# Optimization experiments

Hardware: AMD Instinct MI355X
Metric: run time of the kernel (lower is better)

Reference implementation:

```python
import jax, jax.numpy as jnp
import numpy as np


def bilinear_resize(x, out_h, out_w):
    # x: [B, C, H, W]; matches torch F.interpolate(mode='bilinear', align_corners=False)
    B, C, H, W = x.shape
    ry = jnp.clip((jnp.arange(out_h, dtype=jnp.float32) + 0.5) * (H / out_h) - 0.5, 0.0, H - 1)
    rx = jnp.clip((jnp.arange(out_w, dtype=jnp.float32) + 0.5) * (W / out_w) - 0.5, 0.0, W - 1)
    y0 = jnp.floor(ry).astype(jnp.int32); y1 = jnp.minimum(y0 + 1, H - 1)
    x0 = jnp.floor(rx).astype(jnp.int32); x1 = jnp.minimum(x0 + 1, W - 1)
    wy = (ry - y0)[:, None]  # [out_h,1]
    wx = (rx - x0)[None, :]  # [1,out_w]
    r0 = x[:, :, y0, :]; r1 = x[:, :, y1, :]
    v00 = r0[:, :, :, x0]; v01 = r0[:, :, :, x1]
    v10 = r1[:, :, :, x0]; v11 = r1[:, :, :, x1]
    return (v00 * (1 - wx) + v01 * wx) * (1 - wy) + (v10 * (1 - wx) + v11 * wx) * wy


def setup_inputs() -> dict:
    key0 = jax.random.key(0)
    ks = jax.random.split(key0, 16)
    B, N, C, H = 2, 300, 256, 8
    hw_lvl = np.array([[64, 64], [32, 32], [16, 16]], dtype=np.int64)
    L = int((hw_lvl[:, 0] * hw_lvl[:, 1]).sum())  # 5376
    p = lambda k, sh: (0.02 * jax.random.normal(k, sh, dtype=jnp.float32))
    return {
        'query': jax.random.normal(ks[0], (B, N, C), dtype=jnp.float32),
        'key': jax.random.normal(ks[1], (B, L, C), dtype=jnp.float32),
        'value': jax.random.normal(ks[2], (B, L, C), dtype=jnp.float32),
        'key_padding_mask': jnp.zeros((B, L), dtype=bool),
        'hw_lvl': hw_lvl,
        'Wq': p(ks[3], (C, C)), 'Wk': p(ks[4], (C, C)), 'Wv': p(ks[5], (C, C)),
        'Wp': p(ks[6], (C, C)), 'bp': jnp.zeros((C,), jnp.float32),
        'W1': p(ks[7], (H, H)), 'b1': jnp.zeros((H,), jnp.float32),
        'W2': p(ks[8], (H, H)), 'b2': jnp.zeros((H,), jnp.float32),
        'W3': p(ks[9], (H, H)), 'b3': jnp.zeros((H,), jnp.float32),
        'Wm': p(ks[10], (3 * H, 1)), 'bm': jnp.zeros((1,), jnp.float32),
    }


def reference(query, key, value, key_padding_mask, hw_lvl,
              Wq, Wk, Wv, Wp, bp, W1, b1, W2, b2, W3, b3, Wm, bm):
    hw = np.asarray(hw_lvl)
    h1, wd1 = int(hw[0, 0]), int(hw[0, 1])
    h2, wd2 = int(hw[1, 0]), int(hw[1, 1])
    h3, wd3 = int(hw[2, 0]), int(hw[2, 1])
    w1 = h1 * wd1
    w2 = w1 + h2 * wd2
    B, N, C = query.shape
    L = key.shape[1]
    H = W1.shape[0]
    scale = (C // H) ** -0.5

    q = (query @ Wq).reshape(B, N, H, C // H)
    k = (key @ Wk).reshape(B, L, H, C // H)
    v = (value @ Wv).reshape(B, L, H, C // H)
    attn = jnp.einsum('bnhd,blhd->bhnl', q, k) * scale  # [B,H,N,L]

    ap = attn.transpose(0, 2, 3, 1)  # [B,N,L,H]
    f1 = jax.nn.relu(ap[:, :, :w1] @ W1 + b1)                      # [B,N,w1,H]
    f2 = jax.nn.relu(ap[:, :, w1:w2] @ W2 + b2)                    # [B,N,h2*wd2,H]
    f3 = jax.nn.relu(ap[:, :, w2:] @ W3 + b3)                      # [B,N,h3*wd3,H]
    f2 = f2.transpose(0, 1, 3, 2).reshape(B * N, H, h2, wd2)
    f3 = f3.transpose(0, 1, 3, 2).reshape(B * N, H, h3, wd3)
    f2 = bilinear_resize(f2, h1, wd1).transpose(0, 2, 3, 1).reshape(B, N, w1, H)
    f3 = bilinear_resize(f3, h1, wd1).transpose(0, 2, 3, 1).reshape(B, N, w1, H)
    new_feats = jnp.concatenate([f1, f2, f3], axis=-1)             # [B,N,w1,3H]
    mask = jax.nn.relu(new_feats @ Wm + bm)                        # [B,N,w1,1]

    aw = jax.nn.softmax(attn, axis=-1)                             # [B,H,N,L]
    x = jnp.einsum('bhnl,blhd->bnhd', aw, v).reshape(B, N, C)
    x = x @ Wp + bp
    return x, mask
```

## Files before the change

### kernel.cpp

```cpp
#include <hip/hip_runtime.h>
#include <hip/hip_bf16.h>

typedef __hip_bfloat16 bf16;
typedef __attribute__((ext_vector_type(8))) short short8v;
typedef __attribute__((ext_vector_type(8))) unsigned short ushort8v;
typedef __attribute__((ext_vector_type(4))) unsigned short ushort4v;
typedef __attribute__((ext_vector_type(4))) float float4v;

__device__ __forceinline__ float bfu2f(unsigned short u) {
    union { unsigned int i; float f; } v; v.i = ((unsigned int)u) << 16; return v.f;
}
__device__ __forceinline__ unsigned short f2bfu_rn(float x) {
    union { float f; unsigned int i; } u; u.f = x;
    unsigned int r = (u.i + 0x7FFFu + ((u.i >> 16) & 1u)) >> 16;
    return (unsigned short)r;
}

__global__ __launch_bounds__(256) void cast_wt(
    const float* __restrict__ Wq, const float* __restrict__ Wk,
    const float* __restrict__ Wv, const float* __restrict__ Wp,
    unsigned short* __restrict__ wt)
{
    __shared__ unsigned short tile[64][72];
    const float* W = (blockIdx.z == 0) ? Wq : (blockIdx.z == 1) ? Wk
                   : (blockIdx.z == 2) ? Wv : Wp;
    unsigned short* WT = wt + (size_t)blockIdx.z * 65536;
    const int t = threadIdx.x;
    const int k0 = blockIdx.x * 64, n0 = blockIdx.y * 64;
    {
        const int r = t >> 2, cseg = (t & 3) * 16;
        const float* src = W + (size_t)(k0 + r) * 256 + n0 + cseg;
        #pragma unroll
        for (int j = 0; j < 16; ++j) tile[r][cseg + j] = f2bfu_rn(src[j]);
    }
    __syncthreads();
    {
        const int ch = t & 63, lq = t >> 6;
        ushort8v o0, o1;
        #pragma unroll
        for (int i = 0; i < 8; ++i) o0[i] = tile[lq * 16 + i][ch];
        #pragma unroll
        for (int i = 0; i < 8; ++i) o1[i] = tile[lq * 16 + 8 + i][ch];
        unsigned short* dst = WT + (size_t)(n0 + ch) * 256 + k0 + lq * 16;
        *(ushort8v*)(dst)     = o0;
        *(ushort8v*)(dst + 8) = o1;
    }
}

__device__ __forceinline__ void proj_core(
    const float* __restrict__ aptr, const unsigned short* __restrict__ Wt,
    int nc0, int m16, int quad, float4v acc[8])
{
    #pragma unroll
    for (int i = 0; i < 8; ++i) acc[i] = (float4v){0.f, 0.f, 0.f, 0.f};
    #pragma unroll
    for (int ks = 0; ks < 8; ++ks) {
        float4 a0 = *(const float4*)(aptr + ks * 32);
        float4 a1 = *(const float4*)(aptr + ks * 32 + 4);
        short8v af;
        af[0] = (short)f2bfu_rn(a0.x); af[1] = (short)f2bfu_rn(a0.y);
        af[2] = (short)f2bfu_rn(a0.z); af[3] = (short)f2bfu_rn(a0.w);
        af[4] = (short)f2bfu_rn(a1.x); af[5] = (short)f2bfu_rn(a1.y);
        af[6] = (short)f2bfu_rn(a1.z); af[7] = (short)f2bfu_rn(a1.w);
        #pragma unroll
        for (int i = 0; i < 8; ++i) {
            short8v bfr = *(const short8v*)(Wt + (size_t)(nc0 + i * 16 + m16) * 256 + ks * 32 + quad * 8);
            acc[i] = __builtin_amdgcn_mfma_f32_16x16x32_bf16(af, bfr, acc[i], 0, 0, 0);
        }
    }
}

__global__ __launch_bounds__(256) void proj_all(
    const float* __restrict__ q, const float* __restrict__ k, const float* __restrict__ v,
    const unsigned short* __restrict__ wt,
    unsigned short* __restrict__ qb, unsigned short* __restrict__ kb,
    unsigned short* __restrict__ vt)
{
    const int t = threadIdx.x;
    const int wave = t >> 6, lane = t & 63;
    const int m16 = lane & 15, quad = lane >> 4;
    const int msub = (wave & 1) * 16;
    const int nc0 = (wave >> 1) * 128;
    const int bx = blockIdx.x;

    float4v acc[8];
    if (bx < 19) {
        const int m0 = bx * 32;
        const int arow = min(m0 + msub + m16, 599);
        proj_core(q + (size_t)arow * 256 + quad * 8, wt, nc0, m16, quad, acc);
        #pragma unroll
        for (int i = 0; i < 8; ++i)
            #pragma unroll
            for (int r = 0; r < 4; ++r) {
                int m = m0 + msub + quad * 4 + r;
                if (m < 600)
                    qb[(size_t)m * 256 + nc0 + i * 16 + m16] = f2bfu_rn(acc[i][r]);
            }
    } else if (bx < 355) {
        const int m0 = (bx - 19) * 32;
        proj_core(k + (size_t)(m0 + msub + m16) * 256 + quad * 8, wt + 65536, nc0, m16, quad, acc);
        #pragma unroll
        for (int i = 0; i < 8; ++i)
            #pragma unroll
            for (int r = 0; r < 4; ++r) {
                int m = m0 + msub + quad * 4 + r;
                kb[(size_t)m * 256 + nc0 + i * 16 + m16] = f2bfu_rn(acc[i][r]);
            }
    } else {
        const int m0 = (bx - 355) * 32;
        proj_core(v + (size_t)(m0 + msub + m16) * 256 + quad * 8, wt + 131072, nc0, m16, quad, acc);
        const int bb = (m0 >= 5376) ? 1 : 0;
        const int lcol = m0 - bb * 5376 + msub + quad * 4;
        #pragma unroll
        for (int i = 0; i < 8; ++i) {
            const int ch = nc0 + i * 16 + m16;
            ushort4v p;
            #pragma unroll
            for (int r = 0; r < 4; ++r) p[r] = f2bfu_rn(acc[i][r]);
            *(ushort4v*)(vt + (size_t)(bb * 256 + ch) * 5376 + lcol) = p;
        }
    }
}

__global__ __launch_bounds__(256) void proj_out(
    const float* __restrict__ xb, const unsigned short* __restrict__ Wtp,
    const float* __restrict__ bp, float* __restrict__ out)
{
    const int t = threadIdx.x;
    const int wave = t >> 6, lane = t & 63;
    const int m16 = lane & 15, quad = lane >> 4;
    const int msub = (wave & 1) * 16;
    const int nc0 = (wave >> 1) * 128;
    const int m0 = blockIdx.x * 32;

    const int arow = min(m0 + msub + m16, 599);
    float4v acc[8];
    proj_core(xb + (size_t)arow * 256 + quad * 8, Wtp, nc0, m16, quad, acc);

    #pragma unroll
    for (int i = 0; i < 8; ++i) {
        const float bv = bp[nc0 + i * 16 + m16];
        #pragma unroll
        for (int r = 0; r < 4; ++r) {
            int m = m0 + msub + quad * 4 + r;
            if (m < 600)
                out[(size_t)m * 256 + nc0 + i * 16 + m16] = acc[i][r] + bv;
        }
    }
}

__global__ __launch_bounds__(512) void attn_fused(
    const unsigned short* __restrict__ qb, const unsigned short* __restrict__ kb,
    const unsigned short* __restrict__ vt,
    unsigned short* __restrict__ attn, float* __restrict__ xb)
{
    __shared__ unsigned short probs[8][16 * 232];
    __shared__ float partial[8][64][9];
    __shared__ float SrowP[8][16];

    const int t = threadIdx.x;
    const int wave = t >> 6, lane = t & 63;
    const int n0 = blockIdx.x * 16;
    const int bh = blockIdx.y;
    const int b = bh >> 3, h = bh & 7;
    const int m16 = lane & 15, quad = lane >> 4;
    const float scale = 0.17677669529663687f;

    const unsigned short* qp = qb + (size_t)(b * 300 + min(n0 + m16, 299)) * 256 + h * 32 + quad * 8;
    const short8v qfrag = *(const short8v*)qp;

    const unsigned short* kbase = kb + (size_t)(b * 5376) * 256 + h * 32 + quad * 8;
    const unsigned short* vt0 = vt + (size_t)(b * 256 + h * 32 + m16) * 5376;
    const unsigned short* vt1 = vt0 + (size_t)16 * 5376;

    unsigned short* pw = &probs[wave][0];
    const int lwave = wave * 672;

    float4v c0 = {0.f, 0.f, 0.f, 0.f};
    float4v c1 = {0.f, 0.f, 0.f, 0.f};
    float sm = 0.f;

    for (int cch = 0; cch < 3; ++cch) {
        const int lc = lwave + cch * 224;

        for (int i = 0; i < 14; ++i) {
            const int lcol = lc + i * 16 + m16;
            short8v kf = *(const short8v*)(kbase + (size_t)lcol * 256);
            float4v c = {0.f, 0.f, 0.f, 0.f};
            c = __builtin_amdgcn_mfma_f32_16x16x32_bf16(kf, qfrag, c, 0, 0, 0);
            ushort4v pk;
            #pragma unroll
            for (int r = 0; r < 4; ++r) pk[r] = f2bfu_rn(c[r] * scale);
            *(ushort4v*)(pw + m16 * 232 + i * 16 + quad * 4) = pk;
        }

        {
            const int row = lane >> 2;
            const int n = n0 + row;
            if (n < 300) {
                unsigned short* gdst = attn + ((size_t)(b * 300 + n) * 8 + h) * 5376 + lc;
                const unsigned short* lsrc = pw + row * 232;
                #pragma unroll
                for (int it = 0; it < 7; ++it) {
                    const int colk = (lane & 3) * 8 + it * 32;
                    *(ushort8v*)(gdst + colk) = *(const ushort8v*)(lsrc + colk);
                }
            }
        }

        for (int step = 0; step < 7; ++step) {
            const int lloc = step * 32 + quad * 8;
            ushort8v ua = *(const ushort8v*)(pw + m16 * 232 + lloc);
            short8v af;
            #pragma unroll
            for (int j = 0; j < 8; ++j) {
                float e = __expf(bfu2f(ua[j]));
                sm += e;
                af[j] = (short)f2bfu_rn(e);
            }
            const int lg = lc + lloc;
            short8v b0 = *(const short8v*)(vt0 + lg);
            short8v b1 = *(const short8v*)(vt1 + lg);
            c0 = __builtin_amdgcn_mfma_f32_16x16x32_bf16(af, b0, c0, 0, 0, 0);
            c1 = __builtin_amdgcn_mfma_f32_16x16x32_bf16(af, b1, c1, 0, 0, 0);
        }
    }

    sm += __shfl_xor(sm, 16);
    sm += __shfl_xor(sm, 32);
    if (lane < 16) SrowP[wave][lane] = sm;
    #pragma unroll
    for (int j = 0; j < 4; ++j) {
        partial[wave][lane][j]     = c0[j];
        partial[wave][lane][4 + j] = c1[j];
    }
    __syncthreads();

    if (t < 64) {
        float acc[8] = {0.f, 0.f, 0.f, 0.f, 0.f, 0.f, 0.f, 0.f};
        #pragma unroll
        for (int w = 0; w < 8; ++w)
            #pragma unroll
            for (int j = 0; j < 8; ++j) acc[j] += partial[w][t][j];

        const int d = t & 15, q = t >> 4;
        #pragma unroll
        for (int r = 0; r < 4; ++r) {
            const int row = q * 4 + r;
            const int nn = n0 + row;
            if (nn < 300) {
                float S = 0.f;
                #pragma unroll
                for (int w = 0; w < 8; ++w) S += SrowP[w][row];
                float* o = xb + (size_t)(b * 300 + nn) * 256 + h * 32 + d;
                o[0]  = acc[r] / S;
                o[16] = acc[4 + r] / S;
            }
        }
    }
}

__global__ __launch_bounds__(256) void mask_kernel(
    const bf16* __restrict__ attn,
    const float* __restrict__ W1, const float* __restrict__ b1,
    const float* __restrict__ W2, const float* __restrict__ b2,
    const float* __restrict__ W3, const float* __restrict__ b3,
    const float* __restrict__ Wm, const float* __restrict__ bmp,
    float* __restrict__ out)
{
    __shared__ float g2s[1024];
    __shared__ float g3s[256];
    __shared__ float w1s[64], w2s[64], w3s[64];
    __shared__ float b1s[8], b2s[8], b3s[8];
    __shared__ float wms[24];
    __shared__ float bms;

    const int t  = threadIdx.x;
    const int bn = blockIdx.x;
    const int ph = blockIdx.y;
    const unsigned short* ap = (const unsigned short*)attn + (size_t)bn * 8 * 5376;

    if (t < 64) { w1s[t] = W1[t]; w2s[t] = W2[t]; w3s[t] = W3[t]; }
    if (t < 8)  { b1s[t] = b1[t]; b2s[t] = b2[t]; b3s[t] = b3[t]; }
    if (t < 24) wms[t] = Wm[t];
    if (t == 0) bms = bmp[0];
    __syncthreads();

    {
        const int l2 = t * 4;
        ushort4v u[8];
        #pragma unroll
        for (int hh = 0; hh < 8; ++hh)
            u[hh] = *(const ushort4v*)(ap + hh * 5376 + 4096 + l2);
        #pragma unroll
        for (int pp = 0; pp < 4; ++pp) {
            float g = 0.f;
            #pragma unroll
            for (int hh = 0; hh < 8; ++hh) {
                float s = b2s[hh];
                #pragma unroll
                for (int hp = 0; hp < 8; ++hp) s += bfu2f(u[hp][pp]) * w2s[hp * 8 + hh];
                g += fmaxf(s, 0.f) * wms[8 + hh];
            }
            g2s[l2 + pp] = g;
        }
    }
    if (t < 64) {
        const int l3 = t * 4;
        ushort4v u[8];
        #pragma unroll
        for (int hh = 0; hh < 8; ++hh)
            u[hh] = *(const ushort4v*)(ap + hh * 5376 + 5120 + l3);
        #pragma unroll
        for (int pp = 0; pp < 4; ++pp) {
            float g = 0.f;
            #pragma unroll
            for (int hh = 0; hh < 8; ++hh) {
                float s = b3s[hh];
                #pragma unroll
                for (int hp = 0; hp < 8; ++hp) s += bfu2f(u[hp][pp]) * w3s[hp * 8 + hh];
                g += fmaxf(s, 0.f) * wms[16 + hh];
            }
            g3s[l3 + pp] = g;
        }
    }
    __syncthreads();

    {
        const int p0 = ph * 2048 + t * 8;
        ushort8v u[8];
        #pragma unroll
        for (int hh = 0; hh < 8; ++hh)
            u[hh] = *(const ushort8v*)(ap + hh * 5376 + p0);

        float res[8];
        #pragma unroll
        for (int pp = 0; pp < 8; ++pp) {
            const int p = p0 + pp;
            const int Y = p >> 6, X = p & 63;

            float acc = bms;
            #pragma unroll
            for (int hh = 0; hh < 8; ++hh) {
                float s = b1s[hh];
                #pragma unroll
                for (int hp = 0; hp < 8; ++hp) s += bfu2f(u[hp][pp]) * w1s[hp * 8 + hh];
                acc += fmaxf(s, 0.f) * wms[hh];
            }
            {
                float ry = fminf(fmaxf(0.5f * Y - 0.25f, 0.f), 31.f);
                float rx = fminf(fmaxf(0.5f * X - 0.25f, 0.f), 31.f);
                int y0 = (int)ry, x0 = (int)rx;
                int y1 = min(y0 + 1, 31), x1 = min(x0 + 1, 31);
                float wy = ry - (float)y0, wx = rx - (float)x0;
                acc += (g2s[y0 * 32 + x0] * (1.f - wx) + g2s[y0 * 32 + x1] * wx) * (1.f - wy)
                     + (g2s[y1 * 32 + x0] * (1.f - wx) + g2s[y1 * 32 + x1] * wx) * wy;
            }
            {
                float ry = fminf(fmaxf(0.25f * Y - 0.375f, 0.f), 15.f);
                float rx = fminf(fmaxf(0.25f * X - 0.375f, 0.f), 15.f);
                int y0 = (int)ry, x0 = (int)rx;
                int y1 = min(y0 + 1, 15), x1 = min(x0 + 1, 15);
                float wy = ry - (float)y0, wx = rx - (float)x0;
                acc += (g3s[y0 * 16 + x0] * (1.f - wx) + g3s[y0 * 16 + x1] * wx) * (1.f - wy)
                     + (g3s[y1 * 16 + x0] * (1.f - wx) + g3s[y1 * 16 + x1] * wx) * wy;
            }
            res[pp] = fmaxf(acc, 0.f);
        }
        float* o = out + 153600 + (size_t)bn * 4096 + p0;
        #pragma unroll
        for (int pp = 0; pp < 8; ++pp) o[pp] = res[pp];
    }
}

extern "C" void kernel_launch(void* const* d_in, const int* in_sizes, int n_in,
                              void* d_out, int out_size, void* d_ws, size_t ws_size,
                              hipStream_t stream) {
    const float* query = (const float*)d_in[0];
    const float* key   = (const float*)d_in[1];
    const float* value = (const float*)d_in[2];
    const float* Wq = (const float*)d_in[5];
    const float* Wk = (const float*)d_in[6];
    const float* Wv = (const float*)d_in[7];
    const float* Wp = (const float*)d_in[8];
    const float* bp = (const float*)d_in[9];
    const float* W1 = (const float*)d_in[10];
    const float* b1 = (const float*)d_in[11];
    const float* W2 = (const float*)d_in[12];
    const float* b2 = (const float*)d_in[13];
    const float* W3 = (const float*)d_in[14];
    const float* b3 = (const float*)d_in[15];
    const float* Wm = (const float*)d_in[16];
    const float* bm = (const float*)d_in[17];
    float* out = (float*)d_out;

    char* ws = (char*)d_ws;
    unsigned short* wt = (unsigned short*)(ws);
    bf16*  qb   = (bf16*) (ws + 524288);
    bf16*  kb   = (bf16*) (ws + 831488);
    bf16*  vt   = (bf16*) (ws + 6336512);
    bf16*  attn = (bf16*) (ws + 11841536);
    float* xb   = (float*)(ws + 63451136);

    cast_wt<<<dim3(4, 4, 4), 256, 0, stream>>>(Wq, Wk, Wv, Wp, wt);

    proj_all<<<691, 256, 0, stream>>>(query, key, value, wt,
        (unsigned short*)qb, (unsigned short*)kb, (unsigned short*)vt);

    attn_fused<<<dim3(19, 16), 512, 0, stream>>>(
        (const unsigned short*)qb, (const unsigned short*)kb, (const unsigned short*)vt,
        (unsigned short*)attn, xb);

    mask_kernel<<<dim3(600, 2), 256, 0, stream>>>(attn, W1, b1, W2, b2, W3, b3, Wm, bm, out);

    proj_out<<<19, 256, 0, stream>>>(xb, (const unsigned short*)wt + 196608, bp, out);
}
```

Before: 218.8 us.

## Split attention over key length into three blocks and reduce partials in proj_out

The attention kernel's grid grows from 304 to 912 blocks by splitting the 5376-long key dimension into three z-slices. Each slice writes unnormalized partial outputs and row sums to workspace, and the output projection adds the three partials and divides by the summed row sum before its matmul. This targets low occupancy, since 304 blocks underfill the GPU, at the cost of extra partial-buffer traffic and more work in proj_out. The probability tile row stride also changes from 232 to 236, likely to cut LDS bank conflicts.

```diff
diff --git a/kernel.cpp b/kernel.cpp
--- a/kernel.cpp
+++ b/kernel.cpp
@@ -122,39 +122,12 @@
     }
 }
 
-__global__ __launch_bounds__(256) void proj_out(
-    const float* __restrict__ xb, const unsigned short* __restrict__ Wtp,
-    const float* __restrict__ bp, float* __restrict__ out)
-{
-    const int t = threadIdx.x;
-    const int wave = t >> 6, lane = t & 63;
-    const int m16 = lane & 15, quad = lane >> 4;
-    const int msub = (wave & 1) * 16;
-    const int nc0 = (wave >> 1) * 128;
-    const int m0 = blockIdx.x * 32;
-
-    const int arow = min(m0 + msub + m16, 599);
-    float4v acc[8];
-    proj_core(xb + (size_t)arow * 256 + quad * 8, Wtp, nc0, m16, quad, acc);
-
-    #pragma unroll
-    for (int i = 0; i < 8; ++i) {
-        const float bv = bp[nc0 + i * 16 + m16];
-        #pragma unroll
-        for (int r = 0; r < 4; ++r) {
-            int m = m0 + msub + quad * 4 + r;
-            if (m < 600)
-                out[(size_t)m * 256 + nc0 + i * 16 + m16] = acc[i][r] + bv;
-        }
-    }
-}
-
 __global__ __launch_bounds__(512) void attn_fused(
     const unsigned short* __restrict__ qb, const unsigned short* __restrict__ kb,
     const unsigned short* __restrict__ vt,
-    unsigned short* __restrict__ attn, float* __restrict__ xb)
-{
-    __shared__ unsigned short probs[8][16 * 232];
+    unsigned short* __restrict__ attn, float* __restrict__ xbp, float* __restrict__ Sp)
+{
+    __shared__ unsigned short probs[8][16 * 236];
     __shared__ float partial[8][64][9];
     __shared__ float SrowP[8][16];
 
@@ -162,6 +135,7 @@
     const int wave = t >> 6, lane = t & 63;
     const int n0 = blockIdx.x * 16;
     const int bh = blockIdx.y;
+    const int zz = blockIdx.z;
     const int b = bh >> 3, h = bh & 7;
     const int m16 = lane & 15, quad = lane >> 4;
     const float scale = 0.17677669529663687f;
@@ -174,56 +148,54 @@
     const unsigned short* vt1 = vt0 + (size_t)16 * 5376;
 
     unsigned short* pw = &probs[wave][0];
-    const int lwave = wave * 672;
+    const int lc = zz * 1792 + wave * 224;
 
     float4v c0 = {0.f, 0.f, 0.f, 0.f};
     float4v c1 = {0.f, 0.f, 0.f, 0.f};
     float sm = 0.f;
 
-    for (int cch = 0; cch < 3; ++cch) {
-        const int lc = lwave + cch * 224;
-
-        for (int i = 0; i < 14; ++i) {
-            const int lcol = lc + i * 16 + m16;
-            short8v kf = *(const short8v*)(kbase + (size_t)lcol * 256);
-            float4v c = {0.f, 0.f, 0.f, 0.f};
-            c = __builtin_amdgcn_mfma_f32_16x16x32_bf16(kf, qfrag, c, 0, 0, 0);
-            ushort4v pk;
-            #pragma unroll
-            for (int r = 0; r < 4; ++r) pk[r] = f2bfu_rn(c[r] * scale);
-            *(ushort4v*)(pw + m16 * 232 + i * 16 + quad * 4) = pk;
-        }
-
-        {
-            const int row = lane >> 2;
-            const int n = n0 + row;
-            if (n < 300) {
-                unsigned short* gdst = attn + ((size_t)(b * 300 + n) * 8 + h) * 5376 + lc;
-                const unsigned short* lsrc = pw + row * 232;
-                #pragma unroll
-                for (int it = 0; it < 7; ++it) {
-                    const int colk = (lane & 3) * 8 + it * 32;
-                    *(ushort8v*)(gdst + colk) = *(const ushort8v*)(lsrc + colk);
-                }
-            }
-        }
-
-        for (int step = 0; step < 7; ++step) {
-            const int lloc = step * 32 + quad * 8;
-            ushort8v ua = *(const ushort8v*)(pw + m16 * 232 + lloc);
-            short8v af;
-            #pragma unroll
-            for (int j = 0; j < 8; ++j) {
-                float e = __expf(bfu2f(ua[j]));
-                sm += e;
-                af[j] = (short)f2bfu_rn(e);
-            }
-            const int lg = lc + lloc;
-            short8v b0 = *(const short8v*)(vt0 + lg);
-            short8v b1 = *(const short8v*)(vt1 + lg);
-            c0 = __builtin_amdgcn_mfma_f32_16x16x32_bf16(af, b0, c0, 0, 0, 0);
-            c1 = __builtin_amdgcn_mfma_f32_16x16x32_bf16(af, b1, c1, 0, 0, 0);
-        }
+    #pragma unroll
+    for (int i = 0; i < 14; ++i) {
+        const int lcol = lc + i * 16 + m16;
+        short8v kf = *(const short8v*)(kbase + (size_t)lcol * 256);
+        float4v c = {0.f, 0.f, 0.f, 0.f};
+        c = __builtin_amdgcn_mfma_f32_16x16x32_bf16(kf, qfrag, c, 0, 0, 0);
+        ushort4v pk;
+        #pragma unroll
+        for (int r = 0; r < 4; ++r) pk[r] = f2bfu_rn(c[r] * scale);
+        *(ushort4v*)(pw + m16 * 236 + i * 16 + quad * 4) = pk;
+    }
+
+    {
+        const int row = lane >> 2;
+        const int n = n0 + row;
+        if (n < 300) {
+            unsigned short* gdst = attn + ((size_t)(b * 300 + n) * 8 + h) * 5376 + lc;
+            const unsigned short* lsrc = pw + row * 236;
+            #pragma unroll
+            for (int it = 0; it < 7; ++it) {
+                const int colk = (lane & 3) * 8 + it * 32;
+                *(ushort8v*)(gdst + colk) = *(const ushort8v*)(lsrc + colk);
+            }
+        }
+    }
+
+    #pragma unroll
+    for (int step = 0; step < 7; ++step) {
+        const int lloc = step * 32 + quad * 8;
+        ushort8v ua = *(const ushort8v*)(pw + m16 * 236 + lloc);
+        short8v af;
+        #pragma unroll
+        for (int j = 0; j < 8; ++j) {
+            float e = __expf(bfu2f(ua[j]));
+            sm += e;
+            af[j] = (short)f2bfu_rn(e);
+        }
+        const int lg = lc + lloc;
+        short8v b0 = *(const short8v*)(vt0 + lg);
+        short8v b1 = *(const short8v*)(vt1 + lg);
+        c0 = __builtin_amdgcn_mfma_f32_16x16x32_bf16(af, b0, c0, 0, 0, 0);
+        c1 = __builtin_amdgcn_mfma_f32_16x16x32_bf16(af, b1, c1, 0, 0, 0);
     }
 
     sm += __shfl_xor(sm, 16);
@@ -244,6 +216,8 @@
             for (int j = 0; j < 8; ++j) acc[j] += partial[w][t][j];
 
         const int d = t & 15, q = t >> 4;
+        float* xplane = xbp + (size_t)zz * 153600;
+        float* splane = Sp + (size_t)zz * 4800;
         #pragma unroll
         for (int r = 0; r < 4; ++r) {
             const int row = q * 4 + r;
@@ -252,10 +226,70 @@
                 float S = 0.f;
                 #pragma unroll
                 for (int w = 0; w < 8; ++w) S += SrowP[w][row];
-                float* o = xb + (size_t)(b * 300 + nn) * 256 + h * 32 + d;
-                o[0]  = acc[r] / S;
-                o[16] = acc[4 + r] / S;
-            }
+                if (d == 0) splane[(size_t)(b * 300 + nn) * 8 + h] = S;
+                float* o = xplane + (size_t)(b * 300 + nn) * 256 + h * 32 + d;
+                o[0]  = acc[r];
+                o[16] = acc[4 + r];
+            }
+        }
+    }
+}
+
+__global__ __launch_bounds__(256) void proj_out(
+    const float* __restrict__ xbp, const float* __restrict__ Sp,
+    const unsigned short* __restrict__ Wtp,
+    const float* __restrict__ bp, float* __restrict__ out)
+{
+    const int t = threadIdx.x;
+    const int wave = t >> 6, lane = t & 63;
+    const int m16 = lane & 15, quad = lane >> 4;
+    const int msub = (wave & 1) * 16;
+    const int nc0 = (wave >> 1) * 128;
+    const int m0 = blockIdx.x * 32;
+
+    const int arow = min(m0 + msub + m16, 599);
+    const float* a0p = xbp + (size_t)arow * 256 + quad * 8;
+
+    float4v acc[8];
+    #pragma unroll
+    for (int i = 0; i < 8; ++i) acc[i] = (float4v){0.f, 0.f, 0.f, 0.f};
+
+    #pragma unroll
+    for (int ks = 0; ks < 8; ++ks) {
+        const float S = Sp[(size_t)arow * 8 + ks]
+                      + Sp[4800 + (size_t)arow * 8 + ks]
+                      + Sp[9600 + (size_t)arow * 8 + ks];
+        const float rS = 1.0f / S;
+        float a[8];
+        #pragma unroll
+        for (int half = 0; half < 2; ++half) {
+            const float* p = a0p + ks * 32 + half * 4;
+            float4 x0 = *(const float4*)(p);
+            float4 x1 = *(const float4*)(p + 153600);
+            float4 x2 = *(const float4*)(p + 307200);
+            a[half * 4 + 0] = (x0.x + x1.x + x2.x) * rS;
+            a[half * 4 + 1] = (x0.y + x1.y + x2.y) * rS;
+            a[half * 4 + 2] = (x0.z + x1.z + x2.z) * rS;
+            a[half * 4 + 3] = (x0.w + x1.w + x2.w) * rS;
+        }
+        short8v af;
+        #pragma unroll
+        for (int j = 0; j < 8; ++j) af[j] = (short)f2bfu_rn(a[j]);
+        #pragma unroll
+        for (int i = 0; i < 8; ++i) {
+            short8v bfr = *(const short8v*)(Wtp + (size_t)(nc0 + i * 16 + m16) * 256 + ks * 32 + quad * 8);
+            acc[i] = __builtin_amdgcn_mfma_f32_16x16x32_bf16(af, bfr, acc[i], 0, 0, 0);
+        }
+    }
+
+    #pragma unroll
+    for (int i = 0; i < 8; ++i) {
+        const float bv = bp[nc0 + i * 16 + m16];
+        #pragma unroll
+        for (int r = 0; r < 4; ++r) {
+            int m = m0 + msub + quad * 4 + r;
+            if (m < 600)
+                out[(size_t)m * 256 + nc0 + i * 16 + m16] = acc[i][r] + bv;
         }
     }
 }
@@ -400,18 +434,19 @@
     bf16*  kb   = (bf16*) (ws + 831488);
     bf16*  vt   = (bf16*) (ws + 6336512);
     bf16*  attn = (bf16*) (ws + 11841536);
-    float* xb   = (float*)(ws + 63451136);
+    float* xbp  = (float*)(ws + 63451136);
+    float* Sp   = (float*)(ws + 65294336);
 
     cast_wt<<<dim3(4, 4, 4), 256, 0, stream>>>(Wq, Wk, Wv, Wp, wt);
 
     proj_all<<<691, 256, 0, stream>>>(query, key, value, wt,
         (unsigned short*)qb, (unsigned short*)kb, (unsigned short*)vt);
 
-    attn_fused<<<dim3(19, 16), 512, 0, stream>>>(
+    attn_fused<<<dim3(19, 16, 3), 512, 0, stream>>>(
         (const unsigned short*)qb, (const unsigned short*)kb, (const unsigned short*)vt,
-        (unsigned short*)attn, xb);
+        (unsigned short*)attn, xbp, Sp);
 
     mask_kernel<<<dim3(600, 2), 256, 0, stream>>>(attn, W1, b1, W2, b2, W3, b3, Wm, bm, out);
 
-    proj_out<<<19, 256, 0, stream>>>(xb, (const unsigned short*)wt + 196608, bp, out);
-}
+    proj_out<<<19, 256, 0, stream>>>(xbp, Sp, (const unsigned short*)wt + 196608, bp, out);
+}
```

Result: faster. 210.5 us (-3.8%).
